# Optimization experiments

Measured on AMD Instinct MI355X. Metric: run time of the kernel, lower is better.

## Reference

```python
import jax, jax.numpy as jnp
import numpy as np

S_SAMPLES = 8          # config.ray_samples_per_voxel
T_MIN = 1e-4           # early-termination transmittance threshold


def setup_inputs() -> dict:
    key = jax.random.key(0)
    kp, ks, kd, kc, km, ko, kr = jax.random.split(key, 7)
    V, N = 4096, 4096
    # voxel centers uniform in scene bounds [-1,1]^3
    positions = jax.random.uniform(kp, (V, 3), jnp.float32, -1.0, 1.0)
    # voxel edge lengths: small cubes
    sizes = jax.random.uniform(ks, (V,), jnp.float32, 0.02, 0.08)
    densities = jax.random.normal(kd, (V,), jnp.float32)  # raw, exp-activated
    colors = jax.random.normal(kc, (V, 27), jnp.float32)  # SH deg2: 9*3 coeffs
    morton_codes = jax.random.randint(km, (V,), 0, 16777216, jnp.int32)
    # camera at z=-3 with slight jitter, rays toward the scene
    ray_origins = jnp.tile(jnp.array([0.0, 0.0, -3.0], jnp.float32), (N, 1)) \
        + 0.01 * jax.random.normal(ko, (N, 3), jnp.float32)
    dirs = jax.random.uniform(kr, (N, 3), jnp.float32, -0.4, 0.4)
    dirs = dirs.at[:, 2].set(1.0)
    ray_directions = dirs / jnp.linalg.norm(dirs, axis=1, keepdims=True)
    return {"positions": positions, "sizes": sizes, "densities": densities,
            "colors": colors, "morton_codes": morton_codes,
            "ray_origins": ray_origins, "ray_directions": ray_directions}


def reference(positions, sizes, densities, colors, morton_codes,
              ray_origins, ray_directions):
    # ---- global morton + mean-ray-direction sort ----
    mean_d = ray_directions.mean(axis=0)                       # [3]
    dots = positions @ mean_d                                  # [V]
    keys = morton_codes.astype(jnp.float32) + dots * 1e-6
    order = jnp.argsort(keys)                                  # stable
    pos = positions[order]
    half = (sizes[order] * 0.5)[:, None]                       # [V,1]
    dens_act = jnp.exp(densities[order])                       # 'exp' activation
    col = jax.nn.sigmoid(colors[order][:, :3])                 # dc coeffs, sigmoid

    box_min = pos - half                                       # [V,3]
    box_max = pos + half

    # ---- per-ray slab AABB intersection (vectorized over rays x voxels) ----
    inv_dir = 1.0 / (ray_directions + 1e-8)                    # [N,3]
    o = ray_origins[:, None, :]                                # [N,1,3]
    t1 = (box_min[None, :, :] - o) * inv_dir[:, None, :]       # [N,V,3]
    t2 = (box_max[None, :, :] - o) * inv_dir[:, None, :]
    t_near = jnp.max(jnp.minimum(t1, t2), axis=-1)             # [N,V]
    t_far = jnp.min(jnp.maximum(t1, t2), axis=-1)
    valid = (t_near <= t_far) & (t_far > 0)
    tn = jnp.maximum(t_near, 0.0)

    # ---- per-ray stable sort by entry t (invalid pushed to +inf) ----
    sort_key = jnp.where(valid, tn, jnp.inf)
    idx = jnp.argsort(sort_key, axis=1)                        # [N,V], stable
    tn_s = jnp.take_along_axis(tn, idx, axis=1)
    tf_s = jnp.take_along_axis(t_far, idx, axis=1)
    valid_s = jnp.take_along_axis(valid, idx, axis=1)
    dens_s = dens_act[idx]                                     # [N,V]
    col_s = col[idx]                                           # [N,V,3]

    # ---- sequential alpha compositing via cumprod ----
    dt = (tf_s - tn_s) / S_SAMPLES
    op = 1.0 - jnp.exp(-dens_s * dt)
    op = jnp.where(valid_s, op, 0.0)                           # skipped voxels
    one_m = 1.0 - op
    T_before = jnp.concatenate(
        [jnp.ones_like(op[:, :1]), jnp.cumprod(one_m, axis=1)[:, :-1]], axis=1)
    active = T_before >= T_MIN                                 # early-break mask
    w = jnp.where(active, T_before * op, 0.0)                  # [N,V]

    rgb = jnp.einsum('nv,nvc->nc', w, col_s)                   # [N,3]
    depth = jnp.sum(w * (tn_s + tf_s) * 0.5, axis=1)           # mean of linspace
    final_T = jnp.prod(jnp.where(active, one_m, 1.0), axis=1)
    alpha = 1.0 - final_T
    return rgb, depth, alpha
```

## Files before the change

kernel.cpp:

```cpp
#include <hip/hip_runtime.h>
#include <hip/hip_bf16.h>

#define MAXH 64

__global__ __launch_bounds__(256) void vr_prep(
    const float* __restrict__ positions, const float* __restrict__ sizes,
    const float* __restrict__ densities, const float* __restrict__ colors,
    const int* __restrict__ morton, const float* __restrict__ ray_d,
    float4* __restrict__ P, float* __restrict__ K, float4* __restrict__ C,
    int V, int N)
{
    __shared__ float rx[256], ry[256], rz[256];
    int t = threadIdx.x;
    float sx = 0.f, sy = 0.f, sz = 0.f;
    for (int r = t; r < N; r += 256) {
        sx += ray_d[r*3+0]; sy += ray_d[r*3+1]; sz += ray_d[r*3+2];
    }
    rx[t] = sx; ry[t] = sy; rz[t] = sz;
    __syncthreads();
    for (int s = 128; s > 0; s >>= 1) {
        if (t < s) { rx[t] += rx[t+s]; ry[t] += ry[t+s]; rz[t] += rz[t+s]; }
        __syncthreads();
    }
    float inN = 1.0f / (float)N;
    float mdx = rx[0]*inN, mdy = ry[0]*inN, mdz = rz[0]*inN;

    int v = blockIdx.x * 256 + t;
    if (v < V) {
        float px = positions[v*3+0], py = positions[v*3+1], pz = positions[v*3+2];
        float h = sizes[v] * 0.5f;
        P[v] = make_float4(px, py, pz, h);
        K[v] = (float)morton[v] + (px*mdx + py*mdy + pz*mdz) * 1e-6f;
        float c0 = 1.0f/(1.0f + expf(-colors[v*27+0]));
        float c1 = 1.0f/(1.0f + expf(-colors[v*27+1]));
        float c2 = 1.0f/(1.0f + expf(-colors[v*27+2]));
        C[v] = make_float4(c0, c1, c2, expf(densities[v]));
    }
}

__global__ __launch_bounds__(256) void vr_render(
    const float4* __restrict__ P, const float* __restrict__ K,
    const float4* __restrict__ C,
    const float* __restrict__ ray_o, const float* __restrict__ ray_d,
    float* __restrict__ out, int V, int N)
{
    __shared__ float h_tn[4][MAXH], h_tf[4][MAXH], h_key[4][MAXH];
    __shared__ int   h_v[4][MAXH], s_ord[4][MAXH];
    __shared__ float p_op[4][MAXH], p_c0[4][MAXH], p_c1[4][MAXH],
                     p_c2[4][MAXH], p_mid[4][MAXH];
    __shared__ int   cntL[4];

    int lane = threadIdx.x & 63;
    int w    = threadIdx.x >> 6;
    int ray  = blockIdx.x * 4 + w;

    if (threadIdx.x < 4) cntL[threadIdx.x] = 0;
    __syncthreads();

    if (ray < N) {
        float ox = ray_o[ray*3+0], oy = ray_o[ray*3+1], oz = ray_o[ray*3+2];
        float dx = ray_d[ray*3+0], dy = ray_d[ray*3+1], dz = ray_d[ray*3+2];
        float ix = 1.0f/(dx + 1e-8f), iy = 1.0f/(dy + 1e-8f), iz = 1.0f/(dz + 1e-8f);
        float nox = -ox*ix, noy = -oy*iy, noz = -oz*iz;
        float axx = fabsf(ix), axy = fabsf(iy), axz = fabsf(iz);

        int iters = (V + 127) >> 7;
        for (int k = 0; k < iters; ++k) {
            int v0 = (k << 7) + lane;
            int v1 = v0 + 64;
            float4 pa = (v0 < V) ? P[v0] : make_float4(0,0,0,-1.f);
            float4 pb = (v1 < V) ? P[v1] : make_float4(0,0,0,-1.f);

            #pragma unroll
            for (int u = 0; u < 2; ++u) {
                float4 p = u ? pb : pa;
                int    v = u ? v1 : v0;
                float sx = fmaf(p.x, ix, nox);
                float sy = fmaf(p.y, iy, noy);
                float sz = fmaf(p.z, iz, noz);
                float hx = p.w * axx, hy = p.w * axy, hz = p.w * axz;
                float tnear = fmaxf(fmaxf(sx - hx, sy - hy), sz - hz);
                float tfar  = fminf(fminf(sx + hx, sy + hy), sz + hz);
                if ((tnear <= tfar) && (tfar > 0.0f)) {
                    int slot = atomicAdd(&cntL[w], 1);
                    if (slot < MAXH) {
                        h_tn[w][slot] = fmaxf(tnear, 0.0f);
                        h_tf[w][slot] = tfar;
                        h_v[w][slot]  = v;
                    }
                }
            }
        }
    }
    __syncthreads();
    int m = min(cntL[w], MAXH);

    for (int i = lane; i < m; i += 64) h_key[w][i] = K[h_v[w][i]];
    __syncthreads();

    for (int i = lane; i < m; i += 64) {
        float tni = h_tn[w][i], ki = h_key[w][i];
        int   vi  = h_v[w][i];
        int r = 0;
        for (int j = 0; j < m; ++j) {
            float tnj = h_tn[w][j], kj = h_key[w][j];
            int   vj  = h_v[w][j];
            if ((tnj < tni) || (tnj == tni && ((kj < ki) || (kj == ki && vj < vi)))) r++;
        }
        s_ord[w][r] = i;
    }
    __syncthreads();

    for (int r = lane; r < m; r += 64) {
        int i = s_ord[w][r];
        int v = h_v[w][i];
        float4 c = C[v];
        float tn = h_tn[w][i], tf = h_tf[w][i];
        float dt = (tf - tn) * 0.125f;
        p_op[w][r]  = 1.0f - expf(-c.w * dt);
        p_c0[w][r]  = c.x;  p_c1[w][r] = c.y;  p_c2[w][r] = c.z;
        p_mid[w][r] = (tn + tf) * 0.5f;
    }
    __syncthreads();

    if (lane == 0 && ray < N) {
        float T = 1.0f, r0 = 0.f, r1 = 0.f, r2 = 0.f, dep = 0.f;
        for (int r = 0; r < m; ++r) {
            if (!(T >= 1e-4f)) break;
            float op  = p_op[w][r];
            float wgt = T * op;
            r0  += wgt * p_c0[w][r];
            r1  += wgt * p_c1[w][r];
            r2  += wgt * p_c2[w][r];
            dep += wgt * p_mid[w][r];
            T   *= (1.0f - op);
        }
        out[ray*3 + 0] = r0;
        out[ray*3 + 1] = r1;
        out[ray*3 + 2] = r2;
        out[3*N + ray] = dep;
        out[4*N + ray] = 1.0f - T;
    }
}

extern "C" void kernel_launch(void* const* d_in, const int* in_sizes, int n_in,
                              void* d_out, int out_size, void* d_ws, size_t ws_size,
                              hipStream_t stream)
{
    const float* positions = (const float*)d_in[0];
    const float* sizes     = (const float*)d_in[1];
    const float* densities = (const float*)d_in[2];
    const float* colors    = (const float*)d_in[3];
    const int*   morton    = (const int*)d_in[4];
    const float* ray_o     = (const float*)d_in[5];
    const float* ray_d     = (const float*)d_in[6];
    float* out = (float*)d_out;

    int V = in_sizes[1];
    int N = in_sizes[5] / 3;

    float4* P = (float4*)d_ws;
    float*  K = (float*)(P + V);
    float4* C = (float4*)(K + ((V + 3) & ~3));

    int pblocks = (V + 255) / 256;
    vr_prep<<<pblocks, 256, 0, stream>>>(positions, sizes, densities, colors,
                                         morton, ray_d, P, K, C, V, N);
    int rblocks = (N + 3) / 4;
    vr_render<<<rblocks, 256, 0, stream>>>(P, K, C, ray_o, ray_d, out, V, N);
}
```

Baseline: 88.35 us.

## Share voxel loads across four rays per block in slab intersection

The intersection loop is restructured so each thread tests its voxels against all four rays in the block, instead of each wavefront scanning every voxel for one ray. Each voxel is now loaded once per block rather than once per wavefront, which cuts global/L2 loads fourfold. Per-ray constants are computed by four threads and broadcast through shared memory. Invalid rays get NaN parameters so every test fails. Shared-memory atomics to the per-ray counters now come from all waves, which may raise contention, and the hit-list order changes (the later sort restores it).

```diff
diff --git a/kernel.cpp b/kernel.cpp
--- a/kernel.cpp
+++ b/kernel.cpp
@@ -49,50 +49,69 @@
     __shared__ float p_op[4][MAXH], p_c0[4][MAXH], p_c1[4][MAXH],
                      p_c2[4][MAXH], p_mid[4][MAXH];
     __shared__ int   cntL[4];
+    __shared__ float rp[4][9];
 
-    int lane = threadIdx.x & 63;
-    int w    = threadIdx.x >> 6;
-    int ray  = blockIdx.x * 4 + w;
+    int t    = threadIdx.x;
+    int lane = t & 63;
+    int w    = t >> 6;
 
-    if (threadIdx.x < 4) cntL[threadIdx.x] = 0;
+    if (t < 4) {
+        cntL[t] = 0;
+        int ray = blockIdx.x * 4 + t;
+        if (ray < N) {
+            float ox = ray_o[ray*3+0], oy = ray_o[ray*3+1], oz = ray_o[ray*3+2];
+            float dx = ray_d[ray*3+0], dy = ray_d[ray*3+1], dz = ray_d[ray*3+2];
+            float ix = 1.0f/(dx + 1e-8f), iy = 1.0f/(dy + 1e-8f), iz = 1.0f/(dz + 1e-8f);
+            rp[t][0] = ix;        rp[t][1] = iy;        rp[t][2] = iz;
+            rp[t][3] = -ox*ix;    rp[t][4] = -oy*iy;    rp[t][5] = -oz*iz;
+            rp[t][6] = fabsf(ix); rp[t][7] = fabsf(iy); rp[t][8] = fabsf(iz);
+        } else {
+            float qn = __int_as_float(0x7FC00000);
+            #pragma unroll
+            for (int j = 0; j < 9; ++j) rp[t][j] = qn;
+        }
+    }
     __syncthreads();
 
-    if (ray < N) {
-        float ox = ray_o[ray*3+0], oy = ray_o[ray*3+1], oz = ray_o[ray*3+2];
-        float dx = ray_d[ray*3+0], dy = ray_d[ray*3+1], dz = ray_d[ray*3+2];
-        float ix = 1.0f/(dx + 1e-8f), iy = 1.0f/(dy + 1e-8f), iz = 1.0f/(dz + 1e-8f);
-        float nox = -ox*ix, noy = -oy*iy, noz = -oz*iz;
-        float axx = fabsf(ix), axy = fabsf(iy), axz = fabsf(iz);
+    float ixr[4], iyr[4], izr[4], nxr[4], nyr[4], nzr[4], axr[4], ayr[4], azr[4];
+    #pragma unroll
+    for (int r = 0; r < 4; ++r) {
+        ixr[r] = rp[r][0]; iyr[r] = rp[r][1]; izr[r] = rp[r][2];
+        nxr[r] = rp[r][3]; nyr[r] = rp[r][4]; nzr[r] = rp[r][5];
+        axr[r] = rp[r][6]; ayr[r] = rp[r][7]; azr[r] = rp[r][8];
+    }
 
-        int iters = (V + 127) >> 7;
-        for (int k = 0; k < iters; ++k) {
-            int v0 = (k << 7) + lane;
-            int v1 = v0 + 64;
-            float4 pa = (v0 < V) ? P[v0] : make_float4(0,0,0,-1.f);
-            float4 pb = (v1 < V) ? P[v1] : make_float4(0,0,0,-1.f);
+    for (int v0 = t; v0 < V; v0 += 512) {
+        int v1 = v0 + 256;
+        float4 pa = P[v0];
+        float4 pb = (v1 < V) ? P[v1] : make_float4(0,0,0,-1.f);
 
+        #pragma unroll
+        for (int u = 0; u < 2; ++u) {
+            float4 p = u ? pb : pa;
+            int    v = u ? v1 : v0;
             #pragma unroll
-            for (int u = 0; u < 2; ++u) {
-                float4 p = u ? pb : pa;
-                int    v = u ? v1 : v0;
-                float sx = fmaf(p.x, ix, nox);
-                float sy = fmaf(p.y, iy, noy);
-                float sz = fmaf(p.z, iz, noz);
-                float hx = p.w * axx, hy = p.w * axy, hz = p.w * axz;
-                float tnear = fmaxf(fmaxf(sx - hx, sy - hy), sz - hz);
-                float tfar  = fminf(fminf(sx + hx, sy + hy), sz + hz);
+            for (int r = 0; r < 4; ++r) {
+                float s_x = fmaf(p.x, ixr[r], nxr[r]);
+                float s_y = fmaf(p.y, iyr[r], nyr[r]);
+                float s_z = fmaf(p.z, izr[r], nzr[r]);
+                float hx = p.w * axr[r], hy = p.w * ayr[r], hz = p.w * azr[r];
+                float tnear = fmaxf(fmaxf(s_x - hx, s_y - hy), s_z - hz);
+                float tfar  = fminf(fminf(s_x + hx, s_y + hy), s_z + hz);
                 if ((tnear <= tfar) && (tfar > 0.0f)) {
-                    int slot = atomicAdd(&cntL[w], 1);
+                    int slot = atomicAdd(&cntL[r], 1);
                     if (slot < MAXH) {
-                        h_tn[w][slot] = fmaxf(tnear, 0.0f);
-                        h_tf[w][slot] = tfar;
-                        h_v[w][slot]  = v;
+                        h_tn[r][slot] = fmaxf(tnear, 0.0f);
+                        h_tf[r][slot] = tfar;
+                        h_v[r][slot]  = v;
                     }
                 }
             }
         }
     }
     __syncthreads();
+
+    int ray = blockIdx.x * 4 + w;
     int m = min(cntL[w], MAXH);
 
     for (int i = lane; i < m; i += 64) h_key[w][i] = K[h_v[w][i]];
```

Result: faster. 80.72 us (-8.6%).
